# Optimization experiments

Measured on AMD Instinct MI355X. Metric: run time of the kernel, lower is better.

## Reference

```python
import jax, jax.numpy as jnp
import numpy as np

N_HEADS = 4

def log_cosh(x):
    # numerically stable log(cosh(x)) = |x| + log1p(exp(-2|x|)) - log(2)
    ax = jnp.abs(x)
    return ax + jnp.log1p(jnp.exp(-2.0 * ax)) - jnp.log(2.0)

def setup_inputs() -> dict:
    key = jax.random.key(0)
    ks = jax.random.split(key, 7)
    B, I, A, E, H = 4, 2048, 2048, 256, N_HEADS
    return {
        "query": jax.random.normal(ks[0], (B, I, E), dtype=jnp.float32),
        "key": jax.random.normal(ks[1], (B, A, E), dtype=jnp.float32),
        "value": jax.random.normal(ks[2], (B, A, E), dtype=jnp.float32),
        "distances": jax.random.uniform(ks[3], (B, I, A), dtype=jnp.float32),
        "in_proj_w": jax.random.normal(ks[4], (3 * E, E), dtype=jnp.float32) * 0.05,
        "out_proj_w": jax.random.normal(ks[5], (E, E), dtype=jnp.float32) * 0.05,
        "mass_w": jax.random.normal(ks[6], (H, E), dtype=jnp.float32) * 0.05,
    }

def reference(query, key, value, distances, in_proj_w, out_proj_w, mass_w):
    B, I, E = query.shape
    A = key.shape[1]
    H = N_HEADS
    D = E // H
    # distance-decay additive bias: mass is (B, A, H), nonnegative via log_cosh
    mass = log_cosh(key @ mass_w.T)                       # (B, A, H)
    bias = jnp.einsum('bah,bia->bhia', -mass, distances)  # (B, H, I, A)
    # nn.MultiheadAttention (bias=False) projections
    wq, wk, wv = jnp.split(in_proj_w, 3, axis=0)          # each (E, E)
    q = (query @ wq.T).reshape(B, I, H, D).transpose(0, 2, 1, 3)  # (B,H,I,D)
    k = (key @ wk.T).reshape(B, A, H, D).transpose(0, 2, 1, 3)    # (B,H,A,D)
    v = (value @ wv.T).reshape(B, A, H, D).transpose(0, 2, 1, 3)  # (B,H,A,D)
    scale = 1.0 / jnp.sqrt(jnp.asarray(D, dtype=q.dtype))
    scores = jnp.einsum('bhid,bhad->bhia', q, k) * scale + bias
    attn = jax.nn.softmax(scores, axis=-1)
    o = jnp.einsum('bhia,bhad->bhid', attn, v)            # (B,H,I,D)
    o = o.transpose(0, 2, 1, 3).reshape(B, I, E)
    return o @ out_proj_w.T
```

## Files before the change

### kernel.cpp

```cpp
#include <hip/hip_runtime.h>
#include <hip/hip_bf16.h>
#include <math.h>

#define BB 4
#define II 2048
#define AA 2048
#define EE 256
#define HH 4

#define LOG2E 1.4426950408889634f
#define SCL   (0.125f * LOG2E)

typedef __bf16 bf16_t;
typedef bf16_t bf16x8 __attribute__((ext_vector_type(8)));
typedef bf16_t bf16x4 __attribute__((ext_vector_type(4)));
typedef float  f32x4  __attribute__((ext_vector_type(4)));

static __device__ __forceinline__ f32x4 mfma16(bf16x8 a, bf16x8 b, f32x4 c) {
    return __builtin_amdgcn_mfma_f32_16x16x32_bf16(a, b, c, 0, 0, 0);
}

static __device__ __forceinline__ void glds16(const bf16_t* g, const bf16_t* l) {
    __builtin_amdgcn_global_load_lds(
        (const __attribute__((address_space(1))) void*)g,
        (__attribute__((address_space(3))) void*)l, 16, 0, 0);
}

static __device__ __forceinline__ void proj_body(
    const float* __restrict__ Aop, const float* __restrict__ Bop,
    bf16_t* __restrict__ Cout, int m0, int n0, int TRANS, float cscale,
    bf16_t (*sA)[72], bf16_t (*sB)[72])
{
    const int t = threadIdx.x;
    const int w = t >> 6, l = t & 63, g = l >> 4, q = l & 15;
    const int wm = w >> 1, wn = w & 1;
    const int r = t >> 2, s = t & 3;

    f32x4 acc[2][2] = {};

    for (int kt = 0; kt < 4; ++kt) {
        {
            const float* ga = Aop + (size_t)(m0 + r) * EE + kt * 64 + s * 16;
            float tmp[16];
            *(f32x4*)&tmp[0]  = *(const f32x4*)(ga + 0);
            *(f32x4*)&tmp[4]  = *(const f32x4*)(ga + 4);
            *(f32x4*)&tmp[8]  = *(const f32x4*)(ga + 8);
            *(f32x4*)&tmp[12] = *(const f32x4*)(ga + 12);
            bf16x8 w0, w1;
            #pragma unroll
            for (int i = 0; i < 8; ++i) { w0[i] = (bf16_t)tmp[i]; w1[i] = (bf16_t)tmp[8 + i]; }
            *(bf16x8*)&sA[r][s * 16]     = w0;
            *(bf16x8*)&sA[r][s * 16 + 8] = w1;
        }
        {
            const float* gb = Bop + (size_t)(n0 + r) * EE + kt * 64 + s * 16;
            float tmp[16];
            *(f32x4*)&tmp[0]  = *(const f32x4*)(gb + 0);
            *(f32x4*)&tmp[4]  = *(const f32x4*)(gb + 4);
            *(f32x4*)&tmp[8]  = *(const f32x4*)(gb + 8);
            *(f32x4*)&tmp[12] = *(const f32x4*)(gb + 12);
            bf16x8 w0, w1;
            #pragma unroll
            for (int i = 0; i < 8; ++i) { w0[i] = (bf16_t)tmp[i]; w1[i] = (bf16_t)tmp[8 + i]; }
            *(bf16x8*)&sB[r][s * 16]     = w0;
            *(bf16x8*)&sB[r][s * 16 + 8] = w1;
        }
        __syncthreads();
        #pragma unroll
        for (int ks = 0; ks < 2; ++ks) {
            bf16x8 aA[2], aB[2];
            #pragma unroll
            for (int f = 0; f < 2; ++f) {
                aA[f] = *(const bf16x8*)&sA[wm * 32 + f * 16 + q][ks * 32 + g * 8];
                aB[f] = *(const bf16x8*)&sB[wn * 32 + f * 16 + q][ks * 32 + g * 8];
            }
            #pragma unroll
            for (int fm = 0; fm < 2; ++fm)
            #pragma unroll
            for (int fn = 0; fn < 2; ++fn)
                acc[fm][fn] = mfma16(aA[fm], aB[fn], acc[fm][fn]);
        }
        __syncthreads();
    }
    #pragma unroll
    for (int fm = 0; fm < 2; ++fm)
    #pragma unroll
    for (int fn = 0; fn < 2; ++fn)
    #pragma unroll
    for (int j = 0; j < 4; ++j) {
        const int m = m0 + wm * 32 + fm * 16 + g * 4 + j;
        const int n = n0 + wn * 32 + fn * 16 + q;
        const bf16_t v = (bf16_t)(acc[fm][fn][j] * cscale);
        if (TRANS == 0) {
            Cout[(size_t)m * EE + n] = v;
        } else {
            const int bb = n >> 11, a = n & (AA - 1);
            const int a6 = a & 63;
            const int p6 = (a6 & 32) | ((a6 & 12) << 1) | ((a6 & 16) >> 2) | (a6 & 3);
            Cout[(size_t)bb * (AA * EE) + (size_t)(a >> 6) * (EE * 64) + m * 64 + p6] = v;
        }
    }
}

__global__ __launch_bounds__(256) void fused_pre(
    const float* __restrict__ query, const float* __restrict__ key,
    const float* __restrict__ value, const float* __restrict__ in_w,
    const float* __restrict__ mass_w,
    bf16_t* __restrict__ Qp, bf16_t* __restrict__ Kp, bf16_t* __restrict__ Vt,
    float* __restrict__ massT)
{
    __shared__ __align__(16) bf16_t sA[64][72];
    __shared__ __align__(16) bf16_t sB[64][72];
    const int z = blockIdx.z;
    if (z == 0) {
        proj_body(query, in_w, Qp, blockIdx.x * 64, blockIdx.y * 64, 0, SCL, sA, sB);
    } else if (z == 1) {
        proj_body(key, in_w + 65536, Kp, blockIdx.x * 64, blockIdx.y * 64, 0, 1.0f, sA, sB);
    } else if (z == 2) {
        proj_body(in_w + 131072, value, Vt, blockIdx.y * 64, blockIdx.x * 64, 1, 1.0f, sA, sB);
    } else {
        const int w = threadIdx.x >> 6, l = threadIdx.x & 63;
        const int p = blockIdx.y * 128 + blockIdx.x;
        const int row0 = p * 16 + w * 4;
        f32x4 mw[HH];
        #pragma unroll
        for (int hh = 0; hh < HH; ++hh)
            mw[hh] = *(const f32x4*)(mass_w + hh * EE + l * 4);
        #pragma unroll
        for (int rr = 0; rr < 4; ++rr) {
            const int row = row0 + rr;
            f32x4 kv = *(const f32x4*)(key + (size_t)row * EE + l * 4);
            f32x4 sd;
            #pragma unroll
            for (int hh = 0; hh < HH; ++hh)
                sd[hh] = kv[0]*mw[hh][0] + kv[1]*mw[hh][1] + kv[2]*mw[hh][2] + kv[3]*mw[hh][3];
            #pragma unroll
            for (int off = 32; off >= 1; off >>= 1) {
                #pragma unroll
                for (int hh = 0; hh < HH; ++hh) sd[hh] += __shfl_xor(sd[hh], off, 64);
            }
            if (l == 0) {
                const int bb = row >> 11, a = row & (AA - 1);
                #pragma unroll
                for (int hh = 0; hh < HH; ++hh) {
                    float ax = fabsf(sd[hh]);
                    massT[((size_t)bb * HH + hh) * AA + a] =
                        (ax + log1pf(__expf(-2.0f * ax)) - 0.693147180559945f) * LOG2E;
                }
            }
        }
    }
}

__global__ __launch_bounds__(256) void out_gemm(
    const bf16_t* __restrict__ Aop, const float* __restrict__ Bop,
    float* __restrict__ Cout)
{
    __shared__ __align__(16) bf16_t sA[64][72];
    __shared__ __align__(16) bf16_t sB[64][72];
    const int t = threadIdx.x;
    const int w = t >> 6, l = t & 63, g = l >> 4, q = l & 15;
    const int wm = w >> 1, wn = w & 1;
    const int m0 = blockIdx.x * 64, n0 = blockIdx.y * 64;
    const int r = t >> 2, s = t & 3;

    f32x4 acc[2][2] = {};

    for (int kt = 0; kt < 4; ++kt) {
        {
            const bf16_t* ga = Aop + (size_t)(m0 + r) * EE + kt * 64 + s * 16;
            *(bf16x8*)&sA[r][s * 16]     = *(const bf16x8*)(ga);
            *(bf16x8*)&sA[r][s * 16 + 8] = *(const bf16x8*)(ga + 8);
        }
        {
            const float* gb = Bop + (size_t)(n0 + r) * EE + kt * 64 + s * 16;
            float tmp[16];
            *(f32x4*)&tmp[0]  = *(const f32x4*)(gb + 0);
            *(f32x4*)&tmp[4]  = *(const f32x4*)(gb + 4);
            *(f32x4*)&tmp[8]  = *(const f32x4*)(gb + 8);
            *(f32x4*)&tmp[12] = *(const f32x4*)(gb + 12);
            bf16x8 w0, w1;
            #pragma unroll
            for (int i = 0; i < 8; ++i) { w0[i] = (bf16_t)tmp[i]; w1[i] = (bf16_t)tmp[8 + i]; }
            *(bf16x8*)&sB[r][s * 16]     = w0;
            *(bf16x8*)&sB[r][s * 16 + 8] = w1;
        }
        __syncthreads();
        #pragma unroll
        for (int ks = 0; ks < 2; ++ks) {
            bf16x8 aA[2], aB[2];
            #pragma unroll
            for (int f = 0; f < 2; ++f) {
                aA[f] = *(const bf16x8*)&sA[wm * 32 + f * 16 + q][ks * 32 + g * 8];
                aB[f] = *(const bf16x8*)&sB[wn * 32 + f * 16 + q][ks * 32 + g * 8];
            }
            #pragma unroll
            for (int fm = 0; fm < 2; ++fm)
            #pragma unroll
            for (int fn = 0; fn < 2; ++fn)
                acc[fm][fn] = mfma16(aA[fm], aB[fn], acc[fm][fn]);
        }
        __syncthreads();
    }
    #pragma unroll
    for (int fm = 0; fm < 2; ++fm)
    #pragma unroll
    for (int fn = 0; fn < 2; ++fn)
    #pragma unroll
    for (int j = 0; j < 4; ++j) {
        const int m = m0 + wm * 32 + fm * 16 + g * 4 + j;
        const int n = n0 + wn * 32 + fn * 16 + q;
        Cout[(size_t)m * EE + n] = acc[fm][fn][j];
    }
}

__global__ __launch_bounds__(512, 4) void attn_kernel(
    const bf16_t* __restrict__ Qp, const bf16_t* __restrict__ Kp,
    const bf16_t* __restrict__ Vt, const float* __restrict__ massT,
    const float* __restrict__ dist, bf16_t* __restrict__ Obuf)
{
    __shared__ __align__(16) bf16_t sK[2][2][4096];
    __shared__ __align__(16) bf16_t sV[2][2][4096];
    __shared__ __align__(16) float  sM[2048];

    const int t = threadIdx.x;
    const int wv = t >> 6, l = t & 63, g = l >> 4, q = l & 15;
    const int s = wv >> 2, rg = wv & 3;
    const int h = blockIdx.y, b = blockIdx.z;
    const int i0 = blockIdx.x * 64;

    *(f32x4*)&sM[t * 4] = *(const f32x4*)(massT + ((size_t)b * HH + h) * AA + t * 4);

    bf16x8 qf[2];
    #pragma unroll
    for (int ks = 0; ks < 2; ++ks)
        qf[ks] = *(const bf16x8*)(Qp + (size_t)(b * II + i0 + rg * 16 + q) * EE
                                     + h * 64 + ks * 32 + g * 8);

    const int u0 = rg * 2;
    const int drow0 = u0 * 8 + (l >> 3);
    const int cs = (l & 7) ^ (drow0 & 7);

    const bf16_t* pkg = Kp + ((size_t)b * AA + s * 64 + drow0) * EE + h * 64 + cs * 8;
    const bf16_t* pvg = Vt + (size_t)b * (AA * EE) + (size_t)s * (EE * 64)
                           + (size_t)(h * 64 + drow0) * 64 + cs * 8;
    const float*  pdg = dist + ((size_t)b * II + i0 + rg * 16 + q) * AA + s * 64 + g * 4;

    auto stage = [&](int kb) {
        #pragma unroll
        for (int u = 0; u < 2; ++u) {
            glds16(pkg + u * (8 * EE), &sK[s][kb][(u0 + u) * 512]);
            glds16(pvg + u * (8 * 64), &sV[s][kb][(u0 + u) * 512]);
        }
    };

    f32x4 rd[2][4];

    stage(0);
    pkg += 128 * EE; pvg += 2 * (EE * 64);
    #pragma unroll
    for (int fa = 0; fa < 4; ++fa) rd[0][fa] = *(const f32x4*)(pdg + fa * 16);
    pdg += 128;
    __syncthreads();

    float mrun = -INFINITY;
    f32x4 oacc[4] = {};
    f32x4 lacc = {};
    bf16x8 vone;
    #pragma unroll
    for (int j = 0; j < 8; ++j) vone[j] = (bf16_t)1.0f;

    int ma = s * 64;

    #pragma unroll 2
    for (int k = 0; k < 16; ++k) {
        const int kb = k & 1;
        if (k < 15) {
            stage(kb ^ 1);
            pkg += 128 * EE; pvg += 2 * (EE * 64);
            #pragma unroll
            for (int fa = 0; fa < 4; ++fa)
                rd[(k + 1) & 1][fa] = *(const f32x4*)(pdg + fa * 16);
            pdg += 128;
        }

        f32x4 st[4] = {};
        __builtin_amdgcn_s_setprio(1);
        #pragma unroll
        for (int fa = 0; fa < 4; ++fa) {
            const int row = fa * 16 + q;
            #pragma unroll
            for (int ks = 0; ks < 2; ++ks) {
                bf16x8 ak = *(const bf16x8*)&sK[s][kb][row * 64 + (((ks * 4 + g) ^ (row & 7)) * 8)];
                st[fa] = mfma16(ak, qf[ks], st[fa]);
            }
        }
        __builtin_amdgcn_s_setprio(0);

        float mloc = -INFINITY;
        #pragma unroll
        for (int fa = 0; fa < 4; ++fa) {
            f32x4 ms = *(const f32x4*)&sM[ma + fa * 16 + g * 4];
            #pragma unroll
            for (int j = 0; j < 4; ++j) {
                float sv = fmaf(-ms[j], rd[k & 1][fa][j], st[fa][j]);
                st[fa][j] = sv;
                mloc = fmaxf(mloc, sv);
            }
        }
        ma += 128;

        mloc = fmaxf(mloc, __shfl_xor(mloc, 16, 64));
        mloc = fmaxf(mloc, __shfl_xor(mloc, 32, 64));
        const bool skip = __all(mloc <= mrun + 8.0f);
        float mnew = mrun;
        if (!skip) {
            mnew = fmaxf(mrun, mloc);
            const float sc = exp2f(mrun - mnew);
            mrun = mnew;
            float osc[4];
            #pragma unroll
            for (int j = 0; j < 4; ++j) osc[j] = __shfl(sc, g * 4 + j, 64);
            #pragma unroll
            for (int fd = 0; fd < 4; ++fd)
            #pragma unroll
            for (int j = 0; j < 4; ++j) oacc[fd][j] *= osc[j];
            #pragma unroll
            for (int j = 0; j < 4; ++j) lacc[j] *= osc[j];
        }

        #pragma unroll
        for (int fa = 0; fa < 4; ++fa)
        #pragma unroll
        for (int j = 0; j < 4; ++j)
            st[fa][j] = exp2f(st[fa][j] - mnew);

        bf16x8 pa[2];
        #pragma unroll
        for (int ka = 0; ka < 2; ++ka)
        #pragma unroll
        for (int j = 0; j < 8; ++j)
            pa[ka][j] = (bf16_t)st[2 * ka + (j >> 2)][j & 3];

        __builtin_amdgcn_s_setprio(1);
        #pragma unroll
        for (int ka = 0; ka < 2; ++ka) {
            #pragma unroll
            for (int fd = 0; fd < 4; ++fd) {
                const int row = fd * 16 + q;
                bf16x8 bv = *(const bf16x8*)&sV[s][kb][row * 64 + (((ka * 4 + g) ^ (row & 7)) * 8)];
                oacc[fd] = mfma16(pa[ka], bv, oacc[fd]);
            }
            lacc = mfma16(pa[ka], vone, lacc);
        }
        __builtin_amdgcn_s_setprio(0);

        if (k < 15) {
            __builtin_amdgcn_s_waitcnt(0x0F74);
            __builtin_amdgcn_s_barrier();
        }
    }
    __syncthreads();

    float* cb = (float*)&sK[0][0][0];
    if (s == 1) {
        float* p = cb + (rg * 64 + l) * 24;
        p[0] = mrun;
        *(f32x4*)(p + 4) = lacc;
        #pragma unroll
        for (int fd = 0; fd < 4; ++fd) *(f32x4*)(p + 8 + fd * 4) = oacc[fd];
    }
    __syncthreads();
    if (s == 0) {
        const float* p = cb + (rg * 64 + l) * 24;
        const float mB = p[0];
        const f32x4 lB = *(const f32x4*)(p + 4);
        const float mS = fmaxf(mrun, mB);
        const float aS = exp2f(mrun - mS), bS = exp2f(mB - mS);
        float aSo[4], bSo[4], inv[4];
        #pragma unroll
        for (int j = 0; j < 4; ++j) {
            aSo[j] = __shfl(aS, g * 4 + j, 64);
            bSo[j] = __shfl(bS, g * 4 + j, 64);
        }
        #pragma unroll
        for (int j = 0; j < 4; ++j)
            inv[j] = 1.0f / (lacc[j] * aSo[j] + lB[j] * bSo[j]);
        #pragma unroll
        for (int fd = 0; fd < 4; ++fd) {
            f32x4 ob = *(const f32x4*)(p + 8 + fd * 4);
            #pragma unroll
            for (int j = 0; j < 4; ++j) {
                const float o = (oacc[fd][j] * aSo[j] + ob[j] * bSo[j]) * inv[j];
                Obuf[(size_t)(b * II + i0 + rg * 16 + g * 4 + j) * EE
                     + h * 64 + fd * 16 + q] = (bf16_t)o;
            }
        }
    }
}

extern "C" void kernel_launch(void* const* d_in, const int* in_sizes, int n_in,
                              void* d_out, int out_size, void* d_ws, size_t ws_size,
                              hipStream_t stream)
{
    const float* query  = (const float*)d_in[0];
    const float* key    = (const float*)d_in[1];
    const float* value  = (const float*)d_in[2];
    const float* dist   = (const float*)d_in[3];
    const float* in_w   = (const float*)d_in[4];
    const float* out_w  = (const float*)d_in[5];
    const float* mass_w = (const float*)d_in[6];
    float* out = (float*)d_out;

    char* ws = (char*)d_ws;
    bf16_t* Qp    = (bf16_t*)(ws);
    bf16_t* Kp    = (bf16_t*)(ws + 1 * 4194304);
    bf16_t* Vt    = (bf16_t*)(ws + 2 * 4194304);
    bf16_t* Obuf  = (bf16_t*)(ws + 3 * 4194304);
    float*  massT = (float*) (ws + 4 * 4194304);

    fused_pre<<<dim3(128, 4, 4), dim3(256), 0, stream>>>(
        query, key, value, in_w, mass_w, Qp, Kp, Vt, massT);
    attn_kernel<<<dim3(32, 4, 4), dim3(512), 0, stream>>>(Qp, Kp, Vt, massT, dist, Obuf);
    out_gemm<<<dim3(128, 4), dim3(256), 0, stream>>>(Obuf, out_w, out);
}
```

Measured before the change: 85.54 us.

## Split attention key dimension across four wave groups with 1024-thread blocks

The attention kernel grows from 512 to 1024 threads. Each block now processes the key/value sequence with four split-KV wave groups, each handling 32 keys per step instead of 64, with new swizzled K/V staging and a two-level online-softmax merge at the end. The intent is more waves in flight to hide the latency of streaming the distance matrix and K/V tiles. In exchange it adds a heavier final reduction with extra barriers, uses a full __syncthreads each iteration, and relies on launch bounds of (1024, 8) that may force register spilling.

```diff
diff --git a/kernel.cpp b/kernel.cpp
--- a/kernel.cpp
+++ b/kernel.cpp
@@ -214,14 +214,16 @@
     }
 }
 
-__global__ __launch_bounds__(512, 4) void attn_kernel(
+__global__ __launch_bounds__(1024, 8) void attn_kernel(
     const bf16_t* __restrict__ Qp, const bf16_t* __restrict__ Kp,
     const bf16_t* __restrict__ Vt, const float* __restrict__ massT,
     const float* __restrict__ dist, bf16_t* __restrict__ Obuf)
 {
-    __shared__ __align__(16) bf16_t sK[2][2][4096];
-    __shared__ __align__(16) bf16_t sV[2][2][4096];
-    __shared__ __align__(16) float  sM[2048];
+    __shared__ __align__(16) char smem[73728];
+    bf16_t* sKb = (bf16_t*)smem;
+    bf16_t* sVb = (bf16_t*)(smem + 32768);
+    float*  sM  = (float*)(smem + 65536);
+    float*  cmb = (float*)smem;
 
     const int t = threadIdx.x;
     const int wv = t >> 6, l = t & 63, g = l >> 4, q = l & 15;
@@ -229,7 +231,8 @@
     const int h = blockIdx.y, b = blockIdx.z;
     const int i0 = blockIdx.x * 64;
 
-    *(f32x4*)&sM[t * 4] = *(const f32x4*)(massT + ((size_t)b * HH + h) * AA + t * 4);
+    if (t < 512)
+        *(f32x4*)&sM[t * 4] = *(const f32x4*)(massT + ((size_t)b * HH + h) * AA + t * 4);
 
     bf16x8 qf[2];
     #pragma unroll
@@ -237,29 +240,30 @@
         qf[ks] = *(const bf16x8*)(Qp + (size_t)(b * II + i0 + rg * 16 + q) * EE
                                      + h * 64 + ks * 32 + g * 8);
 
-    const int u0 = rg * 2;
-    const int drow0 = u0 * 8 + (l >> 3);
-    const int cs = (l & 7) ^ (drow0 & 7);
-
-    const bf16_t* pkg = Kp + ((size_t)b * AA + s * 64 + drow0) * EE + h * 64 + cs * 8;
-    const bf16_t* pvg = Vt + (size_t)b * (AA * EE) + (size_t)s * (EE * 64)
-                           + (size_t)(h * 64 + drow0) * 64 + cs * 8;
-    const float*  pdg = dist + ((size_t)b * II + i0 + rg * 16 + q) * AA + s * 64 + g * 4;
+    const int krow = rg * 8 + (l >> 3);
+    const int kcs  = (l & 7) ^ (krow & 7);
+    const int vrow = rg * 16 + (l >> 2);
+    const int vcs  = (l & 3) ^ ((vrow >> 1) & 3);
+
+    const bf16_t* pkg = Kp + ((size_t)b * AA + s * 32 + krow) * EE + h * 64 + kcs * 8;
+    const bf16_t* pvg = Vt + (size_t)b * (AA * EE) + (size_t)(s >> 1) * (EE * 64)
+                           + (size_t)(h * 64 + vrow) * 64 + (s & 1) * 32 + vcs * 8;
+    const float*  pdg = dist + ((size_t)b * II + i0 + rg * 16 + q) * AA + s * 32 + g * 4;
+
+    bf16_t* sKs = sKb + s * 4096;
+    bf16_t* sVs = sVb + s * 4096;
 
     auto stage = [&](int kb) {
-        #pragma unroll
-        for (int u = 0; u < 2; ++u) {
-            glds16(pkg + u * (8 * EE), &sK[s][kb][(u0 + u) * 512]);
-            glds16(pvg + u * (8 * 64), &sV[s][kb][(u0 + u) * 512]);
-        }
+        glds16(pkg, sKs + kb * 2048 + rg * 512);
+        glds16(pvg, sVs + kb * 2048 + rg * 512);
     };
 
-    f32x4 rd[2][4];
+    f32x4 rd[2][2];
 
     stage(0);
     pkg += 128 * EE; pvg += 2 * (EE * 64);
-    #pragma unroll
-    for (int fa = 0; fa < 4; ++fa) rd[0][fa] = *(const f32x4*)(pdg + fa * 16);
+    rd[0][0] = *(const f32x4*)(pdg);
+    rd[0][1] = *(const f32x4*)(pdg + 16);
     pdg += 128;
     __syncthreads();
 
@@ -270,7 +274,7 @@
     #pragma unroll
     for (int j = 0; j < 8; ++j) vone[j] = (bf16_t)1.0f;
 
-    int ma = s * 64;
+    int ma = s * 32;
 
     #pragma unroll 2
     for (int k = 0; k < 16; ++k) {
@@ -278,20 +282,19 @@
         if (k < 15) {
             stage(kb ^ 1);
             pkg += 128 * EE; pvg += 2 * (EE * 64);
-            #pragma unroll
-            for (int fa = 0; fa < 4; ++fa)
-                rd[(k + 1) & 1][fa] = *(const f32x4*)(pdg + fa * 16);
+            rd[(k + 1) & 1][0] = *(const f32x4*)(pdg);
+            rd[(k + 1) & 1][1] = *(const f32x4*)(pdg + 16);
             pdg += 128;
         }
 
-        f32x4 st[4] = {};
+        f32x4 st[2] = {};
         __builtin_amdgcn_s_setprio(1);
         #pragma unroll
-        for (int fa = 0; fa < 4; ++fa) {
+        for (int fa = 0; fa < 2; ++fa) {
             const int row = fa * 16 + q;
             #pragma unroll
             for (int ks = 0; ks < 2; ++ks) {
-                bf16x8 ak = *(const bf16x8*)&sK[s][kb][row * 64 + (((ks * 4 + g) ^ (row & 7)) * 8)];
+                bf16x8 ak = *(const bf16x8*)&sKs[kb * 2048 + row * 64 + (((ks * 4 + g) ^ (row & 7)) * 8)];
                 st[fa] = mfma16(ak, qf[ks], st[fa]);
             }
         }
@@ -299,11 +302,11 @@
 
         float mloc = -INFINITY;
         #pragma unroll
-        for (int fa = 0; fa < 4; ++fa) {
+        for (int fa = 0; fa < 2; ++fa) {
             f32x4 ms = *(const f32x4*)&sM[ma + fa * 16 + g * 4];
             #pragma unroll
             for (int j = 0; j < 4; ++j) {
-                float sv = fmaf(-ms[j], rd[k & 1][fa][j], st[fa][j]);
+                float sv = fmaf(-ms[j], rd[kb][fa][j], st[fa][j]);
                 st[fa][j] = sv;
                 mloc = fmaxf(mloc, sv);
             }
@@ -330,49 +333,71 @@
         }
 
         #pragma unroll
-        for (int fa = 0; fa < 4; ++fa)
+        for (int fa = 0; fa < 2; ++fa)
         #pragma unroll
         for (int j = 0; j < 4; ++j)
             st[fa][j] = exp2f(st[fa][j] - mnew);
 
-        bf16x8 pa[2];
-        #pragma unroll
-        for (int ka = 0; ka < 2; ++ka)
+        bf16x8 pa;
         #pragma unroll
         for (int j = 0; j < 8; ++j)
-            pa[ka][j] = (bf16_t)st[2 * ka + (j >> 2)][j & 3];
+            pa[j] = (bf16_t)st[j >> 2][j & 3];
 
         __builtin_amdgcn_s_setprio(1);
         #pragma unroll
-        for (int ka = 0; ka < 2; ++ka) {
-            #pragma unroll
-            for (int fd = 0; fd < 4; ++fd) {
-                const int row = fd * 16 + q;
-                bf16x8 bv = *(const bf16x8*)&sV[s][kb][row * 64 + (((ka * 4 + g) ^ (row & 7)) * 8)];
-                oacc[fd] = mfma16(pa[ka], bv, oacc[fd]);
-            }
-            lacc = mfma16(pa[ka], vone, lacc);
-        }
+        for (int fd = 0; fd < 4; ++fd) {
+            const int row = fd * 16 + q;
+            bf16x8 bv = *(const bf16x8*)&sVs[kb * 2048 + row * 32 + (((g) ^ ((row >> 1) & 3)) * 8)];
+            oacc[fd] = mfma16(pa, bv, oacc[fd]);
+        }
+        lacc = mfma16(pa, vone, lacc);
         __builtin_amdgcn_s_setprio(0);
 
-        if (k < 15) {
-            __builtin_amdgcn_s_waitcnt(0x0F74);
-            __builtin_amdgcn_s_barrier();
-        }
-    }
-    __syncthreads();
-
-    float* cb = (float*)&sK[0][0][0];
-    if (s == 1) {
-        float* p = cb + (rg * 64 + l) * 24;
+        __syncthreads();
+    }
+
+    const int SLOT = 25;
+    if (s & 1) {
+        float* p = cmb + (((s >> 1) * 4 + rg) * 64 + l) * SLOT;
         p[0] = mrun;
         *(f32x4*)(p + 4) = lacc;
         #pragma unroll
         for (int fd = 0; fd < 4; ++fd) *(f32x4*)(p + 8 + fd * 4) = oacc[fd];
     }
     __syncthreads();
+    if (!(s & 1)) {
+        const float* p = cmb + (((s >> 1) * 4 + rg) * 64 + l) * SLOT;
+        const float mB = p[0];
+        const f32x4 lB = *(const f32x4*)(p + 4);
+        const float mS = fmaxf(mrun, mB);
+        const float aS = exp2f(mrun - mS), bS = exp2f(mB - mS);
+        float aSo[4], bSo[4];
+        #pragma unroll
+        for (int j = 0; j < 4; ++j) {
+            aSo[j] = __shfl(aS, g * 4 + j, 64);
+            bSo[j] = __shfl(bS, g * 4 + j, 64);
+        }
+        #pragma unroll
+        for (int j = 0; j < 4; ++j) lacc[j] = lacc[j] * aSo[j] + lB[j] * bSo[j];
+        #pragma unroll
+        for (int fd = 0; fd < 4; ++fd) {
+            const f32x4 ob = *(const f32x4*)(p + 8 + fd * 4);
+            #pragma unroll
+            for (int j = 0; j < 4; ++j) oacc[fd][j] = oacc[fd][j] * aSo[j] + ob[j] * bSo[j];
+        }
+        mrun = mS;
+    }
+    __syncthreads();
+    if (s == 2) {
+        float* p = cmb + (rg * 64 + l) * SLOT;
+        p[0] = mrun;
+        *(f32x4*)(p + 4) = lacc;
+        #pragma unroll
+        for (int fd = 0; fd < 4; ++fd) *(f32x4*)(p + 8 + fd * 4) = oacc[fd];
+    }
+    __syncthreads();
     if (s == 0) {
-        const float* p = cb + (rg * 64 + l) * 24;
+        const float* p = cmb + (rg * 64 + l) * SLOT;
         const float mB = p[0];
         const f32x4 lB = *(const f32x4*)(p + 4);
         const float mS = fmaxf(mrun, mB);
@@ -388,7 +413,7 @@
             inv[j] = 1.0f / (lacc[j] * aSo[j] + lB[j] * bSo[j]);
         #pragma unroll
         for (int fd = 0; fd < 4; ++fd) {
-            f32x4 ob = *(const f32x4*)(p + 8 + fd * 4);
+            const f32x4 ob = *(const f32x4*)(p + 8 + fd * 4);
             #pragma unroll
             for (int j = 0; j < 4; ++j) {
                 const float o = (oacc[fd][j] * aSo[j] + ob[j] * bSo[j]) * inv[j];
@@ -421,6 +446,6 @@
 
     fused_pre<<<dim3(128, 4, 4), dim3(256), 0, stream>>>(
         query, key, value, in_w, mass_w, Qp, Kp, Vt, massT);
-    attn_kernel<<<dim3(32, 4, 4), dim3(512), 0, stream>>>(Qp, Kp, Vt, massT, dist, Obuf);
+    attn_kernel<<<dim3(32, 4, 4), dim3(1024), 0, stream>>>(Qp, Kp, Vt, massT, dist, Obuf);
     out_gemm<<<dim3(128, 4), dim3(256), 0, stream>>>(Obuf, out_w, out);
 }
```

Result: slower. 222.2 us (+159.8%).

## Drop intra-block KV split in attention kernel, use single 4-wave group

Applied to the files above, without the earlier changes.

The attention kernel previously split the key/value sequence between two 4-wave halves of a 512-thread block and merged their softmax partials through shared memory at the end. It now uses 256 threads that walk all 32 KV tiles sequentially, halving the shared-memory buffers and removing the cross-half merge step. This lowers LDS use and removes the final combine and extra barriers, but halves the waves per block and doubles the serial loop length. With the same grid, there is less parallelism available to hide latency unless more blocks fit per CU.

```diff
diff --git a/kernel.cpp b/kernel.cpp
--- a/kernel.cpp
+++ b/kernel.cpp
@@ -214,22 +214,22 @@
     }
 }
 
-__global__ __launch_bounds__(512, 4) void attn_kernel(
+__global__ __launch_bounds__(256, 4) void attn_kernel(
     const bf16_t* __restrict__ Qp, const bf16_t* __restrict__ Kp,
     const bf16_t* __restrict__ Vt, const float* __restrict__ massT,
     const float* __restrict__ dist, bf16_t* __restrict__ Obuf)
 {
-    __shared__ __align__(16) bf16_t sK[2][2][4096];
-    __shared__ __align__(16) bf16_t sV[2][2][4096];
+    __shared__ __align__(16) bf16_t sK[2][4096];
+    __shared__ __align__(16) bf16_t sV[2][4096];
     __shared__ __align__(16) float  sM[2048];
 
     const int t = threadIdx.x;
-    const int wv = t >> 6, l = t & 63, g = l >> 4, q = l & 15;
-    const int s = wv >> 2, rg = wv & 3;
+    const int rg = t >> 6, l = t & 63, g = l >> 4, q = l & 15;
     const int h = blockIdx.y, b = blockIdx.z;
     const int i0 = blockIdx.x * 64;
 
-    *(f32x4*)&sM[t * 4] = *(const f32x4*)(massT + ((size_t)b * HH + h) * AA + t * 4);
+    *(f32x4*)&sM[t * 8]     = *(const f32x4*)(massT + ((size_t)b * HH + h) * AA + t * 8);
+    *(f32x4*)&sM[t * 8 + 4] = *(const f32x4*)(massT + ((size_t)b * HH + h) * AA + t * 8 + 4);
 
     bf16x8 qf[2];
     #pragma unroll
@@ -241,26 +241,25 @@
     const int drow0 = u0 * 8 + (l >> 3);
     const int cs = (l & 7) ^ (drow0 & 7);
 
-    const bf16_t* pkg = Kp + ((size_t)b * AA + s * 64 + drow0) * EE + h * 64 + cs * 8;
-    const bf16_t* pvg = Vt + (size_t)b * (AA * EE) + (size_t)s * (EE * 64)
-                           + (size_t)(h * 64 + drow0) * 64 + cs * 8;
-    const float*  pdg = dist + ((size_t)b * II + i0 + rg * 16 + q) * AA + s * 64 + g * 4;
+    const bf16_t* pkg = Kp + ((size_t)b * AA + drow0) * EE + h * 64 + cs * 8;
+    const bf16_t* pvg = Vt + (size_t)b * (AA * EE) + (size_t)(h * 64 + drow0) * 64 + cs * 8;
+    const float*  pdg = dist + ((size_t)b * II + i0 + rg * 16 + q) * AA + g * 4;
 
     auto stage = [&](int kb) {
         #pragma unroll
         for (int u = 0; u < 2; ++u) {
-            glds16(pkg + u * (8 * EE), &sK[s][kb][(u0 + u) * 512]);
-            glds16(pvg + u * (8 * 64), &sV[s][kb][(u0 + u) * 512]);
+            glds16(pkg + u * (8 * EE), &sK[kb][(u0 + u) * 512]);
+            glds16(pvg + u * (8 * 64), &sV[kb][(u0 + u) * 512]);
         }
     };
 
     f32x4 rd[2][4];
 
     stage(0);
-    pkg += 128 * EE; pvg += 2 * (EE * 64);
+    pkg += 64 * EE; pvg += EE * 64;
     #pragma unroll
     for (int fa = 0; fa < 4; ++fa) rd[0][fa] = *(const f32x4*)(pdg + fa * 16);
-    pdg += 128;
+    pdg += 64;
     __syncthreads();
 
     float mrun = -INFINITY;
@@ -270,18 +269,18 @@
     #pragma unroll
     for (int j = 0; j < 8; ++j) vone[j] = (bf16_t)1.0f;
 
-    int ma = s * 64;
+    int ma = 0;
 
     #pragma unroll 2
-    for (int k = 0; k < 16; ++k) {
+    for (int k = 0; k < 32; ++k) {
         const int kb = k & 1;
-        if (k < 15) {
+        if (k < 31) {
             stage(kb ^ 1);
-            pkg += 128 * EE; pvg += 2 * (EE * 64);
+            pkg += 64 * EE; pvg += EE * 64;
             #pragma unroll
             for (int fa = 0; fa < 4; ++fa)
                 rd[(k + 1) & 1][fa] = *(const f32x4*)(pdg + fa * 16);
-            pdg += 128;
+            pdg += 64;
         }
 
         f32x4 st[4] = {};
@@ -291,7 +290,7 @@
             const int row = fa * 16 + q;
             #pragma unroll
             for (int ks = 0; ks < 2; ++ks) {
-                bf16x8 ak = *(const bf16x8*)&sK[s][kb][row * 64 + (((ks * 4 + g) ^ (row & 7)) * 8)];
+                bf16x8 ak = *(const bf16x8*)&sK[kb][row * 64 + (((ks * 4 + g) ^ (row & 7)) * 8)];
                 st[fa] = mfma16(ak, qf[ks], st[fa]);
             }
         }
@@ -303,12 +302,12 @@
             f32x4 ms = *(const f32x4*)&sM[ma + fa * 16 + g * 4];
             #pragma unroll
             for (int j = 0; j < 4; ++j) {
-                float sv = fmaf(-ms[j], rd[k & 1][fa][j], st[fa][j]);
+                float sv = fmaf(-ms[j], rd[kb][fa][j], st[fa][j]);
                 st[fa][j] = sv;
                 mloc = fmaxf(mloc, sv);
             }
         }
-        ma += 128;
+        ma += 64;
 
         mloc = fmaxf(mloc, __shfl_xor(mloc, 16, 64));
         mloc = fmaxf(mloc, __shfl_xor(mloc, 32, 64));
@@ -348,54 +347,25 @@
             #pragma unroll
             for (int fd = 0; fd < 4; ++fd) {
                 const int row = fd * 16 + q;
-                bf16x8 bv = *(const bf16x8*)&sV[s][kb][row * 64 + (((ka * 4 + g) ^ (row & 7)) * 8)];
+                bf16x8 bv = *(const bf16x8*)&sV[kb][row * 64 + (((ka * 4 + g) ^ (row & 7)) * 8)];
                 oacc[fd] = mfma16(pa[ka], bv, oacc[fd]);
             }
             lacc = mfma16(pa[ka], vone, lacc);
         }
         __builtin_amdgcn_s_setprio(0);
 
-        if (k < 15) {
-            __builtin_amdgcn_s_waitcnt(0x0F74);
-            __builtin_amdgcn_s_barrier();
-        }
-    }
-    __syncthreads();
-
-    float* cb = (float*)&sK[0][0][0];
-    if (s == 1) {
-        float* p = cb + (rg * 64 + l) * 24;
-        p[0] = mrun;
-        *(f32x4*)(p + 4) = lacc;
-        #pragma unroll
-        for (int fd = 0; fd < 4; ++fd) *(f32x4*)(p + 8 + fd * 4) = oacc[fd];
-    }
-    __syncthreads();
-    if (s == 0) {
-        const float* p = cb + (rg * 64 + l) * 24;
-        const float mB = p[0];
-        const f32x4 lB = *(const f32x4*)(p + 4);
-        const float mS = fmaxf(mrun, mB);
-        const float aS = exp2f(mrun - mS), bS = exp2f(mB - mS);
-        float aSo[4], bSo[4], inv[4];
-        #pragma unroll
-        for (int j = 0; j < 4; ++j) {
-            aSo[j] = __shfl(aS, g * 4 + j, 64);
-            bSo[j] = __shfl(bS, g * 4 + j, 64);
-        }
-        #pragma unroll
-        for (int j = 0; j < 4; ++j)
-            inv[j] = 1.0f / (lacc[j] * aSo[j] + lB[j] * bSo[j]);
-        #pragma unroll
-        for (int fd = 0; fd < 4; ++fd) {
-            f32x4 ob = *(const f32x4*)(p + 8 + fd * 4);
-            #pragma unroll
-            for (int j = 0; j < 4; ++j) {
-                const float o = (oacc[fd][j] * aSo[j] + ob[j] * bSo[j]) * inv[j];
-                Obuf[(size_t)(b * II + i0 + rg * 16 + g * 4 + j) * EE
-                     + h * 64 + fd * 16 + q] = (bf16_t)o;
-            }
-        }
+        __syncthreads();
+    }
+
+    f32x4 inv;
+    #pragma unroll
+    for (int j = 0; j < 4; ++j) inv[j] = 1.0f / lacc[j];
+    #pragma unroll
+    for (int fd = 0; fd < 4; ++fd)
+    #pragma unroll
+    for (int j = 0; j < 4; ++j) {
+        Obuf[(size_t)(b * II + i0 + rg * 16 + g * 4 + j) * EE
+             + h * 64 + fd * 16 + q] = (bf16_t)(oacc[fd][j] * inv[j]);
     }
 }
 
@@ -421,6 +391,6 @@
 
     fused_pre<<<dim3(128, 4, 4), dim3(256), 0, stream>>>(
         query, key, value, in_w, mass_w, Qp, Kp, Vt, massT);
-    attn_kernel<<<dim3(32, 4, 4), dim3(512), 0, stream>>>(Qp, Kp, Vt, massT, dist, Obuf);
+    attn_kernel<<<dim3(32, 4, 4), dim3(256), 0, stream>>>(Qp, Kp, Vt, massT, dist, Obuf);
     out_gemm<<<dim3(128, 4), dim3(256), 0, stream>>>(Obuf, out_w, out);
 }
```

New measurement: 86.74 us. About the same (+1.4%).
